# Optimization experiments

Hardware: AMD Instinct MI355X
Metric: run time of the kernel (lower is better)

## Reference

```python
import jax, jax.numpy as jnp
import numpy as np

L, H, D, HS, DFF, V, B, T = 4, 16, 1024, 64, 5120, 32000, 2, 1024
EPS = 1e-5


def setup_inputs() -> dict:
    key = jax.random.key(0)
    ks = iter(jax.random.split(key, 40))
    def nrm(shape):
        return jax.random.normal(next(ks), shape, dtype=jnp.float32) * 0.02
    inp = {}
    inp['idx'] = jax.random.randint(next(ks), (B, T), 0, V)
    inp['tok_emb'] = nrm((V, D))
    inp['pos_emb'] = nrm((T, D))
    for s in ('u', 'm'):  # u = unmasked heads, m = masked (causal) heads
        inp['Wq_' + s] = nrm((L, H, D, HS)); inp['bq_' + s] = jnp.zeros((L, H, HS), jnp.float32)
        inp['Wk_' + s] = nrm((L, H, D, HS)); inp['bk_' + s] = jnp.zeros((L, H, HS), jnp.float32)
        inp['Wv_' + s] = nrm((L, H, D, HS)); inp['bv_' + s] = jnp.zeros((L, H, HS), jnp.float32)
        inp['Wp_' + s] = nrm((L, D, D));     inp['bp_' + s] = jnp.zeros((L, D), jnp.float32)
    inp['W1'] = nrm((L, D, DFF)); inp['b1'] = jnp.zeros((L, DFF), jnp.float32)
    inp['W2'] = nrm((L, DFF, D)); inp['b2'] = jnp.zeros((L, D), jnp.float32)
    ones = jnp.ones((L, D), jnp.float32); zer = jnp.zeros((L, D), jnp.float32)
    inp['lnf_g'] = ones; inp['lnf_b'] = zer     # LayerNorm inside FeedForward
    inp['n1_g'] = ones;  inp['n1_b'] = zer      # Block.norm1
    inp['n2_g'] = ones;  inp['n2_b'] = zer      # Block.norm2
    inp['nf_g'] = jnp.ones((D,), jnp.float32); inp['nf_b'] = jnp.zeros((D,), jnp.float32)
    inp['Wfin'] = nrm((D, V)); inp['bfin'] = jnp.zeros((V,), jnp.float32)
    return inp


def _ln(x, g, b):
    mu = jnp.mean(x, -1, keepdims=True)
    var = jnp.mean((x - mu) ** 2, -1, keepdims=True)
    return (x - mu) / jnp.sqrt(var + EPS) * g + b


def _attn(xn, Wq, bq, Wk, bk, Wv, bv, Wp, bp, causal):
    # xn: [B,T,D]; Wq/Wk/Wv: [H,D,HS] (all heads batched in one einsum)
    q = jnp.einsum('btd,hde->bhte', xn, Wq) + bq[:, None, :]
    k = jnp.einsum('btd,hde->bhte', xn, Wk) + bk[:, None, :]
    v = jnp.einsum('btd,hde->bhte', xn, Wv) + bv[:, None, :]
    w = jnp.einsum('bhte,bhse->bhts', q, k) * (HS ** -0.5)
    if causal:
        mask = jnp.tril(jnp.ones((w.shape[-2], w.shape[-1]), bool))
        w = jnp.where(mask, w, -jnp.inf)
    w = jax.nn.softmax(w, axis=-1)
    o = jnp.einsum('bhts,bhse->bhte', w, v)
    o = o.transpose(0, 2, 1, 3).reshape(xn.shape[0], xn.shape[1], -1)  # concat heads
    return o @ Wp + bp


def _ffn(x, W1, b1, W2, b2, g, b):
    h = jax.nn.leaky_relu(x @ W1 + b1, negative_slope=0.01)
    return _ln(h @ W2 + b2, g, b)


def reference(idx, tok_emb, pos_emb,
              Wq_u, bq_u, Wk_u, bk_u, Wv_u, bv_u, Wp_u, bp_u,
              Wq_m, bq_m, Wk_m, bk_m, Wv_m, bv_m, Wp_m, bp_m,
              W1, b1, W2, b2, lnf_g, lnf_b, n1_g, n1_b, n2_g, n2_b,
              nf_g, nf_b, Wfin, bfin):
    Tn = idx.shape[1]
    x = tok_emb[idx] + pos_emb[:Tn]
    for l in range(L):
        # exact quirky Block wiring from the original code
        x2 = x + _attn(_ln(x, n1_g[l], n1_b[l]), Wq_u[l], bq_u[l], Wk_u[l], bk_u[l],
                       Wv_u[l], bv_u[l], Wp_u[l], bp_u[l], False)
        x = x2 + _ln(_ffn(_ln(x2, n2_g[l], n2_b[l]), W1[l], b1[l], W2[l], b2[l],
                          lnf_g[l], lnf_b[l]), n1_g[l], n1_b[l])
        x2 = x + _attn(_ln(x, n1_g[l], n1_b[l]), Wq_m[l], bq_m[l], Wk_m[l], bk_m[l],
                       Wv_m[l], bv_m[l], Wp_m[l], bp_m[l], True)
        x = x2 + _ln(_ffn(_ln(x2, n2_g[l], n2_b[l]), W1[l], b1[l], W2[l], b2[l],
                          lnf_g[l], lnf_b[l]), n2_g[l], n2_b[l])
    x = _ln(x, nf_g, nf_b)
    return x @ Wfin + bfin  # logits [B,T,V]; targets=None path -> loss is None
```

## Files before the change

### kernel.cpp

```cpp
#include <hip/hip_runtime.h>
#include <hip/hip_bf16.h>
#include <math.h>

#define LNUM 4
#define H 16
#define D 1024
#define HS 64
#define DFF 5120
#define V 32000
#define BB 2
#define T 1024
#define M (BB*T)
#define EPS 1e-5f

typedef __attribute__((ext_vector_type(8))) short bf16x8;
typedef __attribute__((ext_vector_type(4))) float f32x4;

__device__ __forceinline__ void gload16(const void* g, void* l) {
    __builtin_amdgcn_global_load_lds(
        (const __attribute__((address_space(1))) void*)g,
        (__attribute__((address_space(3))) void*)l, 16, 0, 0);
}

__device__ __forceinline__ float wred_sum(float v) {
    #pragma unroll
    for (int off = 32; off; off >>= 1) v += __shfl_xor(v, off, 64);
    return v;
}

__global__ __launch_bounds__(256) void embed_kernel(const int* __restrict__ idx,
        const float* __restrict__ tok, const float* __restrict__ pos,
        float* __restrict__ x) {
    int row = blockIdx.x;
    int t = row & (T - 1);
    int tok_id = idx[row];
    int c = threadIdx.x * 4;
    float4 a = *(const float4*)&tok[(size_t)tok_id * D + c];
    float4 p = *(const float4*)&pos[(size_t)t * D + c];
    a.x += p.x; a.y += p.y; a.z += p.z; a.w += p.w;
    *(float4*)&x[(size_t)row * D + c] = a;
}

__global__ __launch_bounds__(256) void ln_bf16_w4_kernel(const float* __restrict__ in,
        const float* __restrict__ g, const float* __restrict__ b,
        __hip_bfloat16* __restrict__ out) {
    int w = threadIdx.x >> 6, lane = threadIdx.x & 63;
    int row = blockIdx.x * 4 + w;
    const float* rp = in + (size_t)row * D;
    float4 xv[4];
    float s = 0.f;
    #pragma unroll
    for (int c = 0; c < 4; ++c) {
        xv[c] = *(const float4*)&rp[c * 256 + lane * 4];
        s += xv[c].x + xv[c].y + xv[c].z + xv[c].w;
    }
    float mu = wred_sum(s) * (1.0f / D);
    float vs = 0.f;
    #pragma unroll
    for (int c = 0; c < 4; ++c) {
        xv[c].x -= mu; xv[c].y -= mu; xv[c].z -= mu; xv[c].w -= mu;
        vs += xv[c].x*xv[c].x + xv[c].y*xv[c].y + xv[c].z*xv[c].z + xv[c].w*xv[c].w;
    }
    float rs = rsqrtf(wred_sum(vs) * (1.0f / D) + EPS);
    #pragma unroll
    for (int c = 0; c < 4; ++c) {
        int j = c * 256 + lane * 4;
        float4 gv = *(const float4*)&g[j];
        float4 bv = *(const float4*)&b[j];
        union { ushort4 u4; __hip_bfloat16 h[4]; } pk;
        pk.h[0] = __float2bfloat16(xv[c].x * rs * gv.x + bv.x);
        pk.h[1] = __float2bfloat16(xv[c].y * rs * gv.y + bv.y);
        pk.h[2] = __float2bfloat16(xv[c].z * rs * gv.z + bv.z);
        pk.h[3] = __float2bfloat16(xv[c].w * rs * gv.w + bv.w);
        *(ushort4*)&out[(size_t)row * D + j] = pk.u4;
    }
}

template<int NP>
__global__ __launch_bounds__(256) void ffn_tail_kernel(
        const float* __restrict__ part, const float* __restrict__ b2,
        const float* __restrict__ g1, const float* __restrict__ b1,
        const float* __restrict__ g2, const float* __restrict__ b2g,
        const float* __restrict__ res, float* __restrict__ xout,
        const float* __restrict__ gn, const float* __restrict__ bn,
        __hip_bfloat16* __restrict__ xnout) {
    const size_t MD = (size_t)M * D;
    int w = threadIdx.x >> 6, lane = threadIdx.x & 63;
    int row = blockIdx.x * 4 + w;
    size_t ro = (size_t)row * D;
    float4 f[4];
    float s = 0.f;
    #pragma unroll
    for (int c = 0; c < 4; ++c) {
        int j = c * 256 + lane * 4;
        float4 acc = *(const float4*)&b2[j];
        #pragma unroll
        for (int pI = 0; pI < NP; ++pI) {
            float4 pv = *(const float4*)&part[pI * MD + ro + j];
            acc.x += pv.x; acc.y += pv.y; acc.z += pv.z; acc.w += pv.w;
        }
        f[c] = acc;
        s += acc.x + acc.y + acc.z + acc.w;
    }
    float mu = wred_sum(s) * (1.0f / D);
    float vs = 0.f;
    #pragma unroll
    for (int c = 0; c < 4; ++c) {
        f[c].x -= mu; f[c].y -= mu; f[c].z -= mu; f[c].w -= mu;
        vs += f[c].x*f[c].x + f[c].y*f[c].y + f[c].z*f[c].z + f[c].w*f[c].w;
    }
    float rs = rsqrtf(wred_sum(vs) * (1.0f / D) + EPS);
    float s2 = 0.f;
    #pragma unroll
    for (int c = 0; c < 4; ++c) {
        int j = c * 256 + lane * 4;
        float4 gv = *(const float4*)&g1[j];
        float4 bv = *(const float4*)&b1[j];
        f[c].x = f[c].x * rs * gv.x + bv.x;
        f[c].y = f[c].y * rs * gv.y + bv.y;
        f[c].z = f[c].z * rs * gv.z + bv.z;
        f[c].w = f[c].w * rs * gv.w + bv.w;
        s2 += f[c].x + f[c].y + f[c].z + f[c].w;
    }
    float mu2 = wred_sum(s2) * (1.0f / D);
    float vs2 = 0.f;
    #pragma unroll
    for (int c = 0; c < 4; ++c) {
        f[c].x -= mu2; f[c].y -= mu2; f[c].z -= mu2; f[c].w -= mu2;
        vs2 += f[c].x*f[c].x + f[c].y*f[c].y + f[c].z*f[c].z + f[c].w*f[c].w;
    }
    float rs2 = rsqrtf(wred_sum(vs2) * (1.0f / D) + EPS);
    float s3 = 0.f;
    #pragma unroll
    for (int c = 0; c < 4; ++c) {
        int j = c * 256 + lane * 4;
        float4 gv = *(const float4*)&g2[j];
        float4 bv = *(const float4*)&b2g[j];
        float4 rv = *(const float4*)&res[ro + j];
        f[c].x = rv.x + f[c].x * rs2 * gv.x + bv.x;
        f[c].y = rv.y + f[c].y * rs2 * gv.y + bv.y;
        f[c].z = rv.z + f[c].z * rs2 * gv.z + bv.z;
        f[c].w = rv.w + f[c].w * rs2 * gv.w + bv.w;
        *(float4*)&xout[ro + j] = f[c];
        s3 += f[c].x + f[c].y + f[c].z + f[c].w;
    }
    float mu3 = wred_sum(s3) * (1.0f / D);
    float vs3 = 0.f;
    #pragma unroll
    for (int c = 0; c < 4; ++c) {
        f[c].x -= mu3; f[c].y -= mu3; f[c].z -= mu3; f[c].w -= mu3;
        vs3 += f[c].x*f[c].x + f[c].y*f[c].y + f[c].z*f[c].z + f[c].w*f[c].w;
    }
    float rs3 = rsqrtf(wred_sum(vs3) * (1.0f / D) + EPS);
    #pragma unroll
    for (int c = 0; c < 4; ++c) {
        int j = c * 256 + lane * 4;
        float4 gv = *(const float4*)&gn[j];
        float4 bv = *(const float4*)&bn[j];
        union { ushort4 u4; __hip_bfloat16 h[4]; } pk;
        pk.h[0] = __float2bfloat16(f[c].x * rs3 * gv.x + bv.x);
        pk.h[1] = __float2bfloat16(f[c].y * rs3 * gv.y + bv.y);
        pk.h[2] = __float2bfloat16(f[c].z * rs3 * gv.z + bv.z);
        pk.h[3] = __float2bfloat16(f[c].w * rs3 * gv.w + bv.w);
        *(ushort4*)&xnout[ro + j] = pk.u4;
    }
}

__global__ __launch_bounds__(256) void transpose_bf16_kernel(
        const float* __restrict__ in, __hip_bfloat16* __restrict__ out,
        int R, int C, size_t zin, size_t zout) {
    __shared__ float t[32][33];
    in += (size_t)blockIdx.z * zin; out += (size_t)blockIdx.z * zout;
    int tx = threadIdx.x & 31, ty = threadIdx.x >> 5;
    int c0 = blockIdx.x * 32, r0 = blockIdx.y * 32;
    #pragma unroll
    for (int i = 0; i < 4; ++i)
        t[ty + i * 8][tx] = in[(size_t)(r0 + ty + i * 8) * C + c0 + tx];
    __syncthreads();
    #pragma unroll
    for (int i = 0; i < 4; ++i)
        out[(size_t)(c0 + ty + i * 8) * R + r0 + tx] = __float2bfloat16(t[tx][ty + i * 8]);
}

__global__ __launch_bounds__(256) void transpose_qkv_kernel(
        const float* __restrict__ Wq, const float* __restrict__ Wk,
        const float* __restrict__ Wv, short* __restrict__ outT) {
    __shared__ float t[32][33];
    int z = blockIdx.z;
    int which = z >> 4, h = z & 15;
    const float* in = (which == 0 ? Wq : which == 1 ? Wk : Wv) + (size_t)h * D * HS;
    __hip_bfloat16* out = (__hip_bfloat16*)outT + ((size_t)which * H + h) * HS * D;
    int tx = threadIdx.x & 31, ty = threadIdx.x >> 5;
    int c0 = blockIdx.x * 32, r0 = blockIdx.y * 32;
    #pragma unroll
    for (int i = 0; i < 4; ++i)
        t[ty + i * 8][tx] = in[(size_t)(r0 + ty + i * 8) * HS + c0 + tx];
    __syncthreads();
    #pragma unroll
    for (int i = 0; i < 4; ++i)
        out[(size_t)(c0 + ty + i * 8) * D + r0 + tx] = __float2bfloat16(t[tx][ty + i * 8]);
}

__global__ __launch_bounds__(256) void transpose_v_kernel(const short* __restrict__ in,
        short* __restrict__ out) {
    __shared__ short t[32][33];
    int z = blockIdx.z;
    in  += (size_t)z * T * HS;
    out += (size_t)z * HS * T;
    int tx = threadIdx.x & 31, ty = threadIdx.x >> 5;
    int c0 = blockIdx.x * 32, r0 = blockIdx.y * 32;
    #pragma unroll
    for (int i = 0; i < 4; ++i)
        t[ty + i * 8][tx] = in[(size_t)(r0 + ty + i * 8) * HS + c0 + tx];
    __syncthreads();
    #pragma unroll
    for (int i = 0; i < 4; ++i)
        out[(size_t)(c0 + ty + i * 8) * T + r0 + tx] = t[tx][ty + i * 8];
}

template<int BM, int EPI>
__global__ __launch_bounds__(256) void mm_bf16_kernel(
        const short* __restrict__ A, const short* __restrict__ BT,
        const float* __restrict__ bias0, const float* __restrict__ bias1,
        const float* __restrict__ bias2, const float* __restrict__ res,
        float* __restrict__ C0, float* __restrict__ C1, float* __restrict__ C2,
        __hip_bfloat16* __restrict__ Cbf, int N, int Kloop, int lda) {
    constexpr int BK = 32, BN = 128;
    constexpr int MI = BM / 32;
    __shared__ __align__(16) short As[BM * BK];
    __shared__ __align__(16) short Bs[BN * BK];
    int nwg = gridDim.x * gridDim.y;
    int bid = blockIdx.y * gridDim.x + blockIdx.x;
    int bx = blockIdx.x, by = blockIdx.y;
    if (!(nwg & 7)) {
        int s = (bid & 7) * (nwg >> 3) + (bid >> 3);
        bx = s % gridDim.x; by = s / gridDim.x;
    }
    A  += (size_t)blockIdx.z * Kloop;
    BT += (size_t)blockIdx.z * Kloop;
    int tid = threadIdx.x;
    int lane = tid & 63, wid = tid >> 6;
    int wr = wid >> 1, wc = wid & 1;
    int l15 = lane & 15, l16 = lane >> 4;
    int m0 = by * BM, n0 = bx * BN;
    f32x4 acc[MI][4] = {};
    int sr = tid >> 2, sk = (tid & 3) * 8;
    const short* Ag = A + (size_t)(m0 + sr) * lda + sk;
    const short* Bg = BT + (size_t)(n0 + sr) * lda + sk;
    short* Asl = As + tid * 8;
    short* Bsl = Bs + tid * 8;
    for (int k0 = 0; k0 < Kloop; k0 += BK) {
        #pragma unroll
        for (int i = 0; i < BM / 64; ++i)
            gload16(Ag + k0 + (size_t)(i * 64) * lda, Asl + i * 2048);
        #pragma unroll
        for (int i = 0; i < 2; ++i)
            gload16(Bg + k0 + (size_t)(i * 64) * lda, Bsl + i * 2048);
        __syncthreads();
        bf16x8 af[MI], bfv[4];
        const short* Ab = As + (wr * (BM / 2) + l15) * BK + l16 * 8;
        const short* Bb = Bs + (wc * 64 + l15) * BK + l16 * 8;
        #pragma unroll
        for (int mi = 0; mi < MI; ++mi) af[mi] = *(const bf16x8*)(Ab + mi * 16 * BK);
        #pragma unroll
        for (int ni = 0; ni < 4; ++ni) bfv[ni] = *(const bf16x8*)(Bb + ni * 16 * BK);
        __builtin_amdgcn_s_setprio(1);
        #pragma unroll
        for (int mi = 0; mi < MI; ++mi)
            #pragma unroll
            for (int ni = 0; ni < 4; ++ni)
                acc[mi][ni] = __builtin_amdgcn_mfma_f32_16x16x32_bf16(
                    af[mi], bfv[ni], acc[mi][ni], 0, 0, 0);
        __builtin_amdgcn_s_setprio(0);
        __syncthreads();
    }
    int rbase = m0 + wr * (BM / 2) + l16 * 4;
    int cbase = n0 + wc * 64 + l15;
    size_t zoff = (EPI == 4) ? (size_t)blockIdx.z * 2048 * N : 0;
    #pragma unroll
    for (int mi = 0; mi < MI; ++mi) {
        #pragma unroll
        for (int ni = 0; ni < 4; ++ni) {
            int col = cbase + ni * 16;
            float bv = 0.f;
            if (EPI == 3) {
                int z = col >> 10, nn = col & 1023;
                bv = (z == 0 ? bias0 : z == 1 ? bias1 : bias2)[nn];
            } else if (EPI != 4) bv = bias0[col];
            #pragma unroll
            for (int r = 0; r < 4; ++r) {
                int row = rbase + mi * 16 + r;
                float v = acc[mi][ni][r] + bv;
                if (EPI == 0) {
                    C0[(size_t)row * N + col] = v;
                } else if (EPI == 1) {
                    C0[(size_t)row * N + col] = v + res[(size_t)row * N + col];
                } else if (EPI == 2) {
                    v = v > 0.f ? v : 0.01f * v;
                    Cbf[(size_t)row * N + col] = __float2bfloat16(v);
                } else if (EPI == 4) {
                    C0[zoff + (size_t)row * N + col] = v;
                } else {
                    int z = col >> 10;
                    int hh = (col >> 6) & 15, e = col & 63;
                    int b = row >> 10, t = row & (T - 1);
                    __hip_bfloat16* dst = (__hip_bfloat16*)(z == 0 ? C0 : (z == 1 ? C1 : C2));
                    dst[(((size_t)(b * H + hh)) * T + t) * HS + e] = __float2bfloat16(v);
                }
            }
        }
    }
}

template<int CAUSAL>
__global__ __launch_bounds__(256) void attn_mfma_kernel(
        const short* __restrict__ q, const short* __restrict__ k,
        const short* __restrict__ vt, __hip_bfloat16* __restrict__ att) {
    __shared__ __align__(16) short Ks[64 * 64];
    __shared__ __align__(16) short Vs[64 * 64];
    __shared__ __align__(16) short Ps[4][16 * 64];
    int bh = blockIdx.y;
    int bI = bh >> 4, h = bh & 15;
    int tix = blockIdx.x;
    if (CAUSAL) tix = (tix & 1) ? (15 - (tix >> 1)) : (tix >> 1);
    int t0 = tix * 64;
    int tid = threadIdx.x;
    int lane = tid & 63, w = tid >> 6;
    int l15 = lane & 15, l16 = lane >> 4;

    const short* Qg = q + ((size_t)bh * T + t0 + w * 16 + l15) * HS + l16 * 8;
    bf16x8 qf0 = *(const bf16x8*)Qg;
    bf16x8 qf1 = *(const bf16x8*)(Qg + 32);

    const char* Kg = (const char*)(k + (size_t)bh * T * HS);
    const char* Vg = (const char*)(vt + (size_t)bh * HS * T);

    float m_run[4] = {-1e30f, -1e30f, -1e30f, -1e30f};
    float l_run[4] = {0.f, 0.f, 0.f, 0.f};
    f32x4 acc_o[4] = {};
    short* Pw = Ps[w];
    int pswz = (l15 & 7) << 4;

    int n_tiles = CAUSAL ? (t0 / 64 + 1) : (T / 64);
    for (int it = 0; it < n_tiles; ++it) {
        int s0 = it * 64;
        __syncthreads();
        #pragma unroll
        for (int i = 0; i < 2; ++i) {
            int o = i * 4096 + tid * 16;
            int row = o >> 7, bir = o & 127;
            int sb = bir ^ ((row & 7) << 4);
            gload16(Kg + (size_t)(s0 + row) * 128 + sb, (char*)Ks + o);
            gload16(Vg + (size_t)row * 2048 + s0 * 2 + sb, (char*)Vs + o);
        }
        __syncthreads();

        f32x4 acc_s[4] = {};
        __builtin_amdgcn_s_setprio(1);
        #pragma unroll
        for (int c = 0; c < 4; ++c) {
            int row = c * 16 + l15;
            const char* kb_ = (const char*)Ks + row * 128;
            int swz = (row & 7) << 4;
            bf16x8 kf0 = *(const bf16x8*)(kb_ + ((l16 * 16) ^ swz));
            bf16x8 kf1 = *(const bf16x8*)(kb_ + ((64 + l16 * 16) ^ swz));
            acc_s[c] = __builtin_amdgcn_mfma_f32_16x16x32_bf16(qf0, kf0, acc_s[c], 0, 0, 0);
            acc_s[c] = __builtin_amdgcn_mfma_f32_16x16x32_bf16(qf1, kf1, acc_s[c], 0, 0, 0);
        }
        __builtin_amdgcn_s_setprio(0);

        bool domask = CAUSAL && (it == n_tiles - 1);
        #pragma unroll
        for (int r = 0; r < 4; ++r) {
            float sc[4];
            #pragma unroll
            for (int c = 0; c < 4; ++c) {
                float s = acc_s[c][r];
                if (domask && (s0 + c * 16 + l15) > (t0 + w * 16 + l16 * 4 + r)) s = -1e30f;
                sc[c] = s;
            }
            float tm = fmaxf(fmaxf(sc[0], sc[1]), fmaxf(sc[2], sc[3]));
            tm = fmaxf(tm, __shfl_xor(tm, 1, 16));
            tm = fmaxf(tm, __shfl_xor(tm, 2, 16));
            tm = fmaxf(tm, __shfl_xor(tm, 4, 16));
            tm = fmaxf(tm, __shfl_xor(tm, 8, 16));
            float mn = fmaxf(m_run[r], tm);
            int prow = l16 * 4 + r;
            int pswzr = (prow & 7) << 4;
            float ls = 0.f;
            #pragma unroll
            for (int c = 0; c < 4; ++c) {
                float pv = __expf(0.125f * (sc[c] - mn));
                int pbyte = prow * 128 + (((c * 16 + l15) * 2) ^ pswzr);
                *(__hip_bfloat16*)((char*)Pw + pbyte) = __float2bfloat16(pv);
                ls += pv;
            }
            ls += __shfl_xor(ls, 1, 16);
            ls += __shfl_xor(ls, 2, 16);
            ls += __shfl_xor(ls, 4, 16);
            ls += __shfl_xor(ls, 8, 16);
            float alpha = __expf(0.125f * (m_run[r] - mn));
            l_run[r] = l_run[r] * alpha + ls;
            m_run[r] = mn;
            acc_o[0][r] *= alpha; acc_o[1][r] *= alpha;
            acc_o[2][r] *= alpha; acc_o[3][r] *= alpha;
        }

        const char* Pb = (const char*)Pw + l15 * 128;
        bf16x8 pa0 = *(const bf16x8*)(Pb + ((l16 * 16) ^ pswz));
        bf16x8 pa1 = *(const bf16x8*)(Pb + ((64 + l16 * 16) ^ pswz));
        __builtin_amdgcn_s_setprio(1);
        #pragma unroll
        for (int ni = 0; ni < 4; ++ni) {
            int row = ni * 16 + l15;
            const char* vb_ = (const char*)Vs + row * 128;
            int swz = (row & 7) << 4;
            bf16x8 vf0 = *(const bf16x8*)(vb_ + ((l16 * 16) ^ swz));
            bf16x8 vf1 = *(const bf16x8*)(vb_ + ((64 + l16 * 16) ^ swz));
            acc_o[ni] = __builtin_amdgcn_mfma_f32_16x16x32_bf16(pa0, vf0, acc_o[ni], 0, 0, 0);
            acc_o[ni] = __builtin_amdgcn_mfma_f32_16x16x32_bf16(pa1, vf1, acc_o[ni], 0, 0, 0);
        }
        __builtin_amdgcn_s_setprio(0);
    }

    float inv[4];
    #pragma unroll
    for (int r = 0; r < 4; ++r) inv[r] = 1.0f / l_run[r];
    #pragma unroll
    for (int ni = 0; ni < 4; ++ni) {
        #pragma unroll
        for (int r = 0; r < 4; ++r) {
            size_t orow = ((size_t)(bI * T) + t0 + w * 16 + l16 * 4 + r) * D
                        + h * HS + ni * 16 + l15;
            att[orow] = __float2bfloat16(acc_o[ni][r] * inv[r]);
        }
    }
}

extern "C" void kernel_launch(void* const* d_in, const int* in_sizes, int n_in,
                              void* d_out, int out_size, void* d_ws, size_t ws_size,
                              hipStream_t stream) {
    const int*   idx     = (const int*)d_in[0];
    const float* tok_emb = (const float*)d_in[1];
    const float* pos_emb = (const float*)d_in[2];
    const float* Wq_u = (const float*)d_in[3],  *bq_u = (const float*)d_in[4];
    const float* Wk_u = (const float*)d_in[5],  *bk_u = (const float*)d_in[6];
    const float* Wv_u = (const float*)d_in[7],  *bv_u = (const float*)d_in[8];
    const float* Wp_u = (const float*)d_in[9],  *bp_u = (const float*)d_in[10];
    const float* Wq_m = (const float*)d_in[11], *bq_m = (const float*)d_in[12];
    const float* Wk_m = (const float*)d_in[13], *bk_m = (const float*)d_in[14];
    const float* Wv_m = (const float*)d_in[15], *bv_m = (const float*)d_in[16];
    const float* Wp_m = (const float*)d_in[17], *bp_m = (const float*)d_in[18];
    const float* W1   = (const float*)d_in[19], *b1   = (const float*)d_in[20];
    const float* W2   = (const float*)d_in[21], *b2   = (const float*)d_in[22];
    const float* lnf_g = (const float*)d_in[23], *lnf_b = (const float*)d_in[24];
    const float* n1_g  = (const float*)d_in[25], *n1_b  = (const float*)d_in[26];
    const float* n2_g  = (const float*)d_in[27], *n2_b  = (const float*)d_in[28];
    const float* nf_g  = (const float*)d_in[29], *nf_b  = (const float*)d_in[30];
    const float* Wfin  = (const float*)d_in[31], *bfin  = (const float*)d_in[32];
    float* out = (float*)d_out;

    char* p = (char*)d_ws;
    auto alloc = [&](size_t bytes) { char* r = p; p += (bytes + 255) & ~255ull; return r; };
    float* x    = (float*)alloc((size_t)M * D * 4);
    float* x2   = (float*)alloc((size_t)M * D * 4);
    float* w2p  = (float*)alloc((size_t)4 * M * D * 4);
    short* qbf  = (short*)alloc((size_t)M * D * 2);
    short* kbf  = (short*)alloc((size_t)M * D * 2);
    short* vbf  = (short*)alloc((size_t)M * D * 2);
    short* vtb  = (short*)alloc((size_t)M * D * 2);
    short* xnb  = (short*)alloc((size_t)M * D * 2);
    short* attb = (short*)alloc((size_t)M * D * 2);
    short* hb   = (short*)alloc((size_t)M * DFF * 2);
    short* WqkvT= (short*)alloc((size_t)3 * 1024 * 1024 * 2);
    short* WpT  = (short*)alloc((size_t)1024 * 1024 * 2);
    short* W1T  = (short*)alloc((size_t)D * DFF * 2);
    short* W2T  = (short*)alloc((size_t)DFF * D * 2);
    short* WfT  = (short*)alloc((size_t)D * V * 2);

    embed_kernel<<<M, 256, 0, stream>>>(idx, tok_emb, pos_emb, x);
    ln_bf16_w4_kernel<<<M / 4, 256, 0, stream>>>(x, n1_g, n1_b, (__hip_bfloat16*)xnb);
    transpose_bf16_kernel<<<dim3(V / 32, D / 32, 1), 256, 0, stream>>>(
        Wfin, (__hip_bfloat16*)WfT, D, V, 0, 0);

    for (int l = 0; l < LNUM; ++l) {
        const float *n1g = n1_g + l * D, *n1b = n1_b + l * D;
        const float *n2g = n2_g + l * D, *n2b = n2_b + l * D;
        const float *lfg = lnf_g + l * D, *lfb = lnf_b + l * D;
        const float *W1l = W1 + (size_t)l * D * DFF, *b1l = b1 + l * DFF;
        const float *W2l = W2 + (size_t)l * DFF * D, *b2l = b2 + l * D;
        transpose_bf16_kernel<<<dim3(DFF / 32, D / 32, 1), 256, 0, stream>>>(
            W1l, (__hip_bfloat16*)W1T, D, DFF, 0, 0);
        transpose_bf16_kernel<<<dim3(D / 32, DFF / 32, 1), 256, 0, stream>>>(
            W2l, (__hip_bfloat16*)W2T, DFF, D, 0, 0);
        for (int half = 0; half < 2; ++half) {
            const float *Wq_, *bq_, *Wk_, *bk_, *Wv_, *bv_, *Wp_, *bp_;
            if (half == 0) { Wq_ = Wq_u; bq_ = bq_u; Wk_ = Wk_u; bk_ = bk_u;
                             Wv_ = Wv_u; bv_ = bv_u; Wp_ = Wp_u; bp_ = bp_u; }
            else           { Wq_ = Wq_m; bq_ = bq_m; Wk_ = Wk_m; bk_ = bk_m;
                             Wv_ = Wv_m; bv_ = bv_m; Wp_ = Wp_m; bp_ = bp_m; }
            Wq_ += (size_t)l * H * D * HS;  bq_ += l * H * HS;
            Wk_ += (size_t)l * H * D * HS;  bk_ += l * H * HS;
            Wv_ += (size_t)l * H * D * HS;  bv_ += l * H * HS;
            Wp_ += (size_t)l * D * D;       bp_ += l * D;

            transpose_qkv_kernel<<<dim3(HS / 32, D / 32, 48), 256, 0, stream>>>(
                Wq_, Wk_, Wv_, WqkvT);
            transpose_bf16_kernel<<<dim3(D / 32, D / 32, 1), 256, 0, stream>>>(
                Wp_, (__hip_bfloat16*)WpT, D, D, 0, 0);

            mm_bf16_kernel<128, 3><<<dim3(3072 / 128, M / 128), 256, 0, stream>>>(
                xnb, WqkvT, bq_, bk_, bv_, nullptr,
                (float*)qbf, (float*)kbf, (float*)vbf, nullptr, 3072, D, D);
            transpose_v_kernel<<<dim3(HS / 32, T / 32, BB * H), 256, 0, stream>>>(vbf, vtb);
            if (half == 0)
                attn_mfma_kernel<0><<<dim3(T / 64, BB * H), 256, 0, stream>>>(
                    qbf, kbf, vtb, (__hip_bfloat16*)attb);
            else
                attn_mfma_kernel<1><<<dim3(T / 64, BB * H), 256, 0, stream>>>(
                    qbf, kbf, vtb, (__hip_bfloat16*)attb);
            mm_bf16_kernel<64, 1><<<dim3(D / 128, M / 64), 256, 0, stream>>>(
                attb, WpT, bp_, nullptr, nullptr, x, x2, nullptr, nullptr, nullptr, D, D, D);
            ln_bf16_w4_kernel<<<M / 4, 256, 0, stream>>>(x2, n2g, n2b, (__hip_bfloat16*)xnb);
            mm_bf16_kernel<128, 2><<<dim3(DFF / 128, M / 128), 256, 0, stream>>>(
                xnb, W1T, b1l, nullptr, nullptr, nullptr, nullptr, nullptr, nullptr,
                (__hip_bfloat16*)hb, DFF, D, D);
            mm_bf16_kernel<128, 4><<<dim3(D / 128, M / 128, 4), 256, 0, stream>>>(
                hb, W2T, nullptr, nullptr, nullptr, nullptr, w2p, nullptr, nullptr,
                nullptr, D, DFF / 4, DFF);
            const float* og = half ? n2g : n1g;
            const float* ob = half ? n2b : n1b;
            const float* gn; const float* bn;
            if (half == 0)      { gn = n1g; bn = n1b; }
            else if (l < LNUM-1){ gn = n1_g + (l+1)*D; bn = n1_b + (l+1)*D; }
            else                { gn = nf_g; bn = nf_b; }
            ffn_tail_kernel<4><<<M / 4, 256, 0, stream>>>(
                w2p, b2l, lfg, lfb, og, ob, x2, x, gn, bn, (__hip_bfloat16*)xnb);
        }
    }
    mm_bf16_kernel<128, 0><<<dim3(V / 128, M / 128), 256, 0, stream>>>(
        xnb, WfT, bfin, nullptr, nullptr, nullptr, out, nullptr, nullptr, nullptr, V, D, D);
}
```

Before: 1.750 ms.

## Widen attention key tiles to 128 and transpose GEMM grid block mapping

The attention kernel now processes 128 keys per iteration instead of 64. This halves the number of loop iterations and their barriers, and changes the K/V/P LDS swizzles to match the wider rows. Separately, every GEMM launch swaps grid dimensions so blockIdx.x walks M tiles, which changes which blocks run together and share weight tiles in cache. The wider tile raises LDS use and register pressure. It also makes causal masking coarser at the diagonal, so more masked work is done there.

```diff
diff --git a/kernel.cpp b/kernel.cpp
--- a/kernel.cpp
+++ b/kernel.cpp
@@ -242,7 +242,7 @@
     int lane = tid & 63, wid = tid >> 6;
     int wr = wid >> 1, wc = wid & 1;
     int l15 = lane & 15, l16 = lane >> 4;
-    int m0 = by * BM, n0 = bx * BN;
+    int m0 = bx * BM, n0 = by * BN;
     f32x4 acc[MI][4] = {};
     int sr = tid >> 2, sk = (tid & 3) * 8;
     const short* Ag = A + (size_t)(m0 + sr) * lda + sk;
@@ -276,7 +276,7 @@
     }
     int rbase = m0 + wr * (BM / 2) + l16 * 4;
     int cbase = n0 + wc * 64 + l15;
-    size_t zoff = (EPI == 4) ? (size_t)blockIdx.z * 2048 * N : 0;
+    size_t zoff = (EPI == 4) ? (size_t)blockIdx.z * M * N : 0;
     #pragma unroll
     for (int mi = 0; mi < MI; ++mi) {
         #pragma unroll
@@ -316,9 +316,9 @@
 __global__ __launch_bounds__(256) void attn_mfma_kernel(
         const short* __restrict__ q, const short* __restrict__ k,
         const short* __restrict__ vt, __hip_bfloat16* __restrict__ att) {
-    __shared__ __align__(16) short Ks[64 * 64];
-    __shared__ __align__(16) short Vs[64 * 64];
-    __shared__ __align__(16) short Ps[4][16 * 64];
+    __shared__ __align__(16) short Ks[128 * 64];
+    __shared__ __align__(16) short Vs[64 * 128];
+    __shared__ __align__(16) short Ps[4][16 * 128];
     int bh = blockIdx.y;
     int bI = bh >> 4, h = bh & 15;
     int tix = blockIdx.x;
@@ -338,27 +338,33 @@
     float m_run[4] = {-1e30f, -1e30f, -1e30f, -1e30f};
     float l_run[4] = {0.f, 0.f, 0.f, 0.f};
     f32x4 acc_o[4] = {};
-    short* Pw = Ps[w];
-    int pswz = (l15 & 7) << 4;
-
-    int n_tiles = CAUSAL ? (t0 / 64 + 1) : (T / 64);
+    char* Pw = (char*)Ps[w];
+    int pswz = l15 << 4;
+
+    int n_tiles = CAUSAL ? (t0 / 128 + 1) : (T / 128);
     for (int it = 0; it < n_tiles; ++it) {
-        int s0 = it * 64;
+        int s0 = it * 128;
         __syncthreads();
         #pragma unroll
-        for (int i = 0; i < 2; ++i) {
+        for (int i = 0; i < 4; ++i) {
             int o = i * 4096 + tid * 16;
             int row = o >> 7, bir = o & 127;
-            int sb = bir ^ ((row & 7) << 4);
-            gload16(Kg + (size_t)(s0 + row) * 128 + sb, (char*)Ks + o);
-            gload16(Vg + (size_t)row * 2048 + s0 * 2 + sb, (char*)Vs + o);
+            gload16(Kg + (size_t)(s0 + row) * 128 + (bir ^ ((row & 7) << 4)),
+                    (char*)Ks + o);
+        }
+        #pragma unroll
+        for (int i = 0; i < 4; ++i) {
+            int o = i * 4096 + tid * 16;
+            int row = o >> 8, bb = o & 255;
+            gload16(Vg + (size_t)row * 2048 + s0 * 2 + (bb ^ ((row & 15) << 4)),
+                    (char*)Vs + o);
         }
         __syncthreads();
 
-        f32x4 acc_s[4] = {};
+        f32x4 acc_s[8] = {};
         __builtin_amdgcn_s_setprio(1);
         #pragma unroll
-        for (int c = 0; c < 4; ++c) {
+        for (int c = 0; c < 8; ++c) {
             int row = c * 16 + l15;
             const char* kb_ = (const char*)Ks + row * 128;
             int swz = (row & 7) << 4;
@@ -372,27 +378,28 @@
         bool domask = CAUSAL && (it == n_tiles - 1);
         #pragma unroll
         for (int r = 0; r < 4; ++r) {
-            float sc[4];
+            float sc[8];
             #pragma unroll
-            for (int c = 0; c < 4; ++c) {
+            for (int c = 0; c < 8; ++c) {
                 float s = acc_s[c][r];
                 if (domask && (s0 + c * 16 + l15) > (t0 + w * 16 + l16 * 4 + r)) s = -1e30f;
                 sc[c] = s;
             }
-            float tm = fmaxf(fmaxf(sc[0], sc[1]), fmaxf(sc[2], sc[3]));
+            float tm = fmaxf(fmaxf(fmaxf(sc[0], sc[1]), fmaxf(sc[2], sc[3])),
+                             fmaxf(fmaxf(sc[4], sc[5]), fmaxf(sc[6], sc[7])));
             tm = fmaxf(tm, __shfl_xor(tm, 1, 16));
             tm = fmaxf(tm, __shfl_xor(tm, 2, 16));
             tm = fmaxf(tm, __shfl_xor(tm, 4, 16));
             tm = fmaxf(tm, __shfl_xor(tm, 8, 16));
             float mn = fmaxf(m_run[r], tm);
             int prow = l16 * 4 + r;
-            int pswzr = (prow & 7) << 4;
+            int pswzr = prow << 4;
             float ls = 0.f;
             #pragma unroll
-            for (int c = 0; c < 4; ++c) {
+            for (int c = 0; c < 8; ++c) {
                 float pv = __expf(0.125f * (sc[c] - mn));
-                int pbyte = prow * 128 + (((c * 16 + l15) * 2) ^ pswzr);
-                *(__hip_bfloat16*)((char*)Pw + pbyte) = __float2bfloat16(pv);
+                int pbyte = prow * 256 + (((c * 16 + l15) * 2) ^ pswzr);
+                *(__hip_bfloat16*)(Pw + pbyte) = __float2bfloat16(pv);
                 ls += pv;
             }
             ls += __shfl_xor(ls, 1, 16);
@@ -406,19 +413,22 @@
             acc_o[2][r] *= alpha; acc_o[3][r] *= alpha;
         }
 
-        const char* Pb = (const char*)Pw + l15 * 128;
-        bf16x8 pa0 = *(const bf16x8*)(Pb + ((l16 * 16) ^ pswz));
-        bf16x8 pa1 = *(const bf16x8*)(Pb + ((64 + l16 * 16) ^ pswz));
+        const char* Pb = Pw + l15 * 256;
+        bf16x8 pa[4];
+        #pragma unroll
+        for (int t = 0; t < 4; ++t)
+            pa[t] = *(const bf16x8*)(Pb + ((t * 64 + l16 * 16) ^ pswz));
         __builtin_amdgcn_s_setprio(1);
         #pragma unroll
         for (int ni = 0; ni < 4; ++ni) {
             int row = ni * 16 + l15;
-            const char* vb_ = (const char*)Vs + row * 128;
-            int swz = (row & 7) << 4;
-            bf16x8 vf0 = *(const bf16x8*)(vb_ + ((l16 * 16) ^ swz));
-            bf16x8 vf1 = *(const bf16x8*)(vb_ + ((64 + l16 * 16) ^ swz));
-            acc_o[ni] = __builtin_amdgcn_mfma_f32_16x16x32_bf16(pa0, vf0, acc_o[ni], 0, 0, 0);
-            acc_o[ni] = __builtin_amdgcn_mfma_f32_16x16x32_bf16(pa1, vf1, acc_o[ni], 0, 0, 0);
+            const char* vb_ = (const char*)Vs + row * 256;
+            int swz = (row & 15) << 4;
+            #pragma unroll
+            for (int t = 0; t < 4; ++t) {
+                bf16x8 vf = *(const bf16x8*)(vb_ + ((t * 64 + l16 * 16) ^ swz));
+                acc_o[ni] = __builtin_amdgcn_mfma_f32_16x16x32_bf16(pa[t], vf, acc_o[ni], 0, 0, 0);
+            }
         }
         __builtin_amdgcn_s_setprio(0);
     }
@@ -509,7 +519,7 @@
             transpose_bf16_kernel<<<dim3(D / 32, D / 32, 1), 256, 0, stream>>>(
                 Wp_, (__hip_bfloat16*)WpT, D, D, 0, 0);
 
-            mm_bf16_kernel<128, 3><<<dim3(3072 / 128, M / 128), 256, 0, stream>>>(
+            mm_bf16_kernel<128, 3><<<dim3(M / 128, 3072 / 128), 256, 0, stream>>>(
                 xnb, WqkvT, bq_, bk_, bv_, nullptr,
                 (float*)qbf, (float*)kbf, (float*)vbf, nullptr, 3072, D, D);
             transpose_v_kernel<<<dim3(HS / 32, T / 32, BB * H), 256, 0, stream>>>(vbf, vtb);
@@ -519,13 +529,13 @@
             else
                 attn_mfma_kernel<1><<<dim3(T / 64, BB * H), 256, 0, stream>>>(
                     qbf, kbf, vtb, (__hip_bfloat16*)attb);
-            mm_bf16_kernel<64, 1><<<dim3(D / 128, M / 64), 256, 0, stream>>>(
+            mm_bf16_kernel<64, 1><<<dim3(M / 64, D / 128), 256, 0, stream>>>(
                 attb, WpT, bp_, nullptr, nullptr, x, x2, nullptr, nullptr, nullptr, D, D, D);
             ln_bf16_w4_kernel<<<M / 4, 256, 0, stream>>>(x2, n2g, n2b, (__hip_bfloat16*)xnb);
-            mm_bf16_kernel<128, 2><<<dim3(DFF / 128, M / 128), 256, 0, stream>>>(
+            mm_bf16_kernel<128, 2><<<dim3(M / 128, DFF / 128), 256, 0, stream>>>(
                 xnb, W1T, b1l, nullptr, nullptr, nullptr, nullptr, nullptr, nullptr,
                 (__hip_bfloat16*)hb, DFF, D, D);
-            mm_bf16_kernel<128, 4><<<dim3(D / 128, M / 128, 4), 256, 0, stream>>>(
+            mm_bf16_kernel<128, 4><<<dim3(M / 128, D / 128, 4), 256, 0, stream>>>(
                 hb, W2T, nullptr, nullptr, nullptr, nullptr, w2p, nullptr, nullptr,
                 nullptr, D, DFF / 4, DFF);
             const float* og = half ? n2g : n1g;
@@ -538,6 +548,6 @@
                 w2p, b2l, lfg, lfb, og, ob, x2, x, gn, bn, (__hip_bfloat16*)xnb);
         }
     }
-    mm_bf16_kernel<128, 0><<<dim3(V / 128, M / 128), 256, 0, stream>>>(
+    mm_bf16_kernel<128, 0><<<dim3(M / 128, V / 128), 256, 0, stream>>>(
         xnb, WfT, bfin, nullptr, nullptr, nullptr, out, nullptr, nullptr, nullptr, V, D, D);
 }
```

Result: faster. 1.707 ms (-2.4%).
